# Performance work log

Hardware: AMD Instinct MI355X
Metric: run time of the kernel (lower is better)

The kernel has to match this reference:

```python
import jax, jax.numpy as jnp
import numpy as np

NUM_HEADS = 4
LN_EPS = 1e-5
L2_EPS = 1e-12


def setup_inputs() -> dict:
    key = jax.random.key(0)
    ks = jax.random.split(key, 10)
    B, L, D, Hd = 256, 197, 768, 512
    dh = Hd // NUM_HEADS  # 128
    NC = 1000
    sc = lambda k, shape, s: jax.random.normal(k, shape, jnp.float32) * s
    return {
        "cls_token": jax.random.normal(ks[0], (B, D), jnp.float32),
        "x": jax.random.normal(ks[1], (B, L, D), jnp.float32),
        "proj_w": sc(ks[2], (D, Hd), 0.02),
        "proj_b": jnp.zeros((Hd,), jnp.float32),
        "ln_g": jnp.ones((dh,), jnp.float32),
        "ln_b": jnp.zeros((dh,), jnp.float32),
        "conv1_w": sc(ks[3], (3, 3, 3, 3), 0.2),
        "conv2_w": sc(ks[4], (3, 3, 3, 3), 0.2),
        "cls1_w": sc(ks[5], (D, NC), 0.02),
        "cls1_b": jnp.zeros((NC,), jnp.float32),
        "cls2_w": sc(ks[6], (2883, NC), 0.02),
        "cls2_b": jnp.zeros((NC,), jnp.float32),
    }


def reference(cls_token, x, proj_w, proj_b, ln_g, ln_b, conv1_w, conv2_w,
              cls1_w, cls1_b, cls2_w, cls2_b):
    B, L, D = x.shape
    dh = ln_g.shape[0]
    # proj on patch tokens (drop cls at position 0)
    xp = x[:, 1:, :] @ proj_w + proj_b            # (B, 196, 512)
    Lp = xp.shape[1]
    H = xp.shape[2] // dh
    heads = xp.reshape(B, Lp, H, dh).transpose(2, 0, 1, 3)  # (H, B, Lp, dh)
    # LayerNorm over last dim (eps=1e-5, biased var, affine)
    mu = heads.mean(-1, keepdims=True)
    var = heads.var(-1, keepdims=True)
    hn = (heads - mu) * jax.lax.rsqrt(var + LN_EPS) * ln_g + ln_b
    # Covariance._remove_mean: adaptive_avg_pool2d on (B, dh, Lp) -> mean over BOTH dh and Lp per sample
    hn = hn - hn.mean(axis=(2, 3), keepdims=True)
    # 'near' cross-covariances between adjacent heads, all pairs batched
    x1, x2 = hn[:-1], hn[1:]                      # (H-1, B, Lp, dh)
    cov = jnp.einsum('pbnd,pbne->pbde', x1, x2) / Lp  # (H-1, B, dh, dh)
    # L2 normalize over dim=2 (row axis of each dh x dh map), F.normalize eps
    nrm = jnp.sqrt(jnp.sum(cov * cov, axis=2, keepdims=True))
    cov = cov / jnp.maximum(nrm, L2_EPS)
    cov = cov.transpose(1, 0, 2, 3)               # (B, 3, 128, 128)
    conv = lambda z, w: jax.lax.conv_general_dilated(
        z, w, (2, 2), 'VALID', dimension_numbers=('NCHW', 'OIHW', 'NCHW'))
    z = conv(cov, conv1_w)                        # (B, 3, 63, 63)
    z = jax.nn.gelu(z, approximate=False)
    z = conv(z, conv2_w)                          # (B, 3, 31, 31)
    flat = z.reshape(B, -1)                       # (B, 2883)
    out = ((cls_token @ cls1_w + cls1_b) + (flat @ cls2_w + cls2_b)) / 2
    return out
```

## Files before the change

### kernel.cpp

```cpp
#include <hip/hip_runtime.h>
#include <hip/hip_bf16.h>
#include <cstdint>

typedef __bf16 bf16_t;
typedef __bf16 bf16x4 __attribute__((ext_vector_type(4)));
typedef __bf16 bf16x8 __attribute__((ext_vector_type(8)));
typedef float floatx4 __attribute__((ext_vector_type(4)));

#define LNEPS 1e-5f

__device__ inline void async_copy16(const bf16_t* g, bf16_t* l) {
    __builtin_amdgcn_global_load_lds((const __attribute__((address_space(1))) void*)g,
                                     (__attribute__((address_space(3))) void*)l,
                                     16, 0, 0);
}

__global__ __launch_bounds__(256)
void k_transpose_w(const float* __restrict__ w, bf16_t* __restrict__ wt) {
    __shared__ bf16_t tile[32][33];
    const int bx = blockIdx.x;
    const int by = blockIdx.y;
    const int tx = threadIdx.x & 31, ty = threadIdx.x >> 5;
    for (int i = ty; i < 32; i += 8)
        tile[i][tx] = (bf16_t)w[(by*32 + i)*512 + bx*32 + tx];
    __syncthreads();
    for (int i = ty; i < 32; i += 8)
        wt[(bx*32 + i)*768 + by*32 + tx] = tile[tx][i];
}

__global__ __launch_bounds__(256, 3)
void k_proj_ln(const float* __restrict__ x, const bf16_t* __restrict__ wt,
               const float* __restrict__ pb, const float* __restrict__ lng,
               const float* __restrict__ lnb, bf16_t* __restrict__ hn,
               float* __restrict__ csum)
{
    __shared__ bf16_t As[2][128*32];
    __shared__ bf16_t Bs[2][128*32];

    const int t = threadIdx.x;
    const int lane = t & 63;
    const int wv = t >> 6;
    const int q = lane >> 4;
    const int c = lane & 15;
    const int h  = blockIdx.x;
    const int m0 = blockIdx.y * 128;

    const int arow = t >> 1;
    const int acol = (t & 1) * 16;
    const int agm  = m0 + arow;
    const int ab   = agm / 196;
    const int al   = agm - ab * 196;
    const float* ag = x + ((long)(ab * 197 + al + 1) * 768) + acol;

    const int srow  = t >> 2;
    const int skoff = (t & 3) * 8;
    const bf16_t* bg = wt + (h*128 + srow) * 768 + skoff;

    floatx4 acc[2][8];
#pragma unroll
    for (int i = 0; i < 2; i++)
#pragma unroll
        for (int j = 0; j < 8; j++)
#pragma unroll
            for (int r = 0; r < 4; r++) acc[i][j][r] = 0.f;

    floatx4 a0 = *(const floatx4*)(ag);
    floatx4 a1 = *(const floatx4*)(ag + 4);
    floatx4 a2 = *(const floatx4*)(ag + 8);
    floatx4 a3 = *(const floatx4*)(ag + 12);
    async_copy16(bg,          &Bs[0][t*8]);
    async_copy16(bg + 64*768, &Bs[0][2048 + t*8]);
    {
        bf16x8 w0, w1;
#pragma unroll
        for (int e = 0; e < 4; e++) {
            w0[e] = (bf16_t)a0[e]; w0[e+4] = (bf16_t)a1[e];
            w1[e] = (bf16_t)a2[e]; w1[e+4] = (bf16_t)a3[e];
        }
        *(bf16x8*)&As[0][arow*32 + acol]     = w0;
        *(bf16x8*)&As[0][arow*32 + acol + 8] = w1;
    }
    __syncthreads();

    int buf = 0;
    for (int ks = 0; ks < 24; ks++) {
        const int nbuf = buf ^ 1;
        if (ks < 23) {
            const int kn = (ks + 1) * 32;
            a0 = *(const floatx4*)(ag + kn);
            a1 = *(const floatx4*)(ag + kn + 4);
            a2 = *(const floatx4*)(ag + kn + 8);
            a3 = *(const floatx4*)(ag + kn + 12);
            async_copy16(bg + kn,          &Bs[nbuf][t*8]);
            async_copy16(bg + 64*768 + kn, &Bs[nbuf][2048 + t*8]);
        }
        bf16x8 af[2], bfr[8];
#pragma unroll
        for (int i = 0; i < 2; i++)
            af[i] = *(const bf16x8*)&As[buf][(wv*32 + i*16 + c)*32 + q*8];
#pragma unroll
        for (int j = 0; j < 8; j++)
            bfr[j] = *(const bf16x8*)&Bs[buf][(j*16 + c)*32 + q*8];
#pragma unroll
        for (int i = 0; i < 2; i++)
#pragma unroll
            for (int j = 0; j < 8; j++)
                acc[i][j] = __builtin_amdgcn_mfma_f32_16x16x32_bf16(af[i], bfr[j], acc[i][j], 0, 0, 0);
        if (ks < 23) {
            bf16x8 w0, w1;
#pragma unroll
            for (int e = 0; e < 4; e++) {
                w0[e] = (bf16_t)a0[e]; w0[e+4] = (bf16_t)a1[e];
                w1[e] = (bf16_t)a2[e]; w1[e+4] = (bf16_t)a3[e];
            }
            *(bf16x8*)&As[nbuf][arow*32 + acol]     = w0;
            *(bf16x8*)&As[nbuf][arow*32 + acol + 8] = w1;
        }
        __syncthreads();
        buf = nbuf;
    }

    float bias[8], gg[8], bb[8];
#pragma unroll
    for (int j = 0; j < 8; j++) {
        const int d = j*16 + c;
        bias[j] = pb[h*128 + d];
        gg[j]   = lng[d];
        bb[j]   = lnb[d];
    }
    float cs0[8], cs1[8];
#pragma unroll
    for (int j = 0; j < 8; j++) { cs0[j] = 0.f; cs1[j] = 0.f; }
    const int b0 = m0 / 196;
    const int bL = (m0 + 127) / 196;
#pragma unroll
    for (int i = 0; i < 2; i++) {
#pragma unroll
        for (int r = 0; r < 4; r++) {
            float s = 0.f, s2 = 0.f;
#pragma unroll
            for (int j = 0; j < 8; j++) {
                const float v = acc[i][j][r] + bias[j];
                acc[i][j][r] = v;
                s += v; s2 += v*v;
            }
#pragma unroll
            for (int o = 1; o < 16; o <<= 1) { s += __shfl_xor(s, o); s2 += __shfl_xor(s2, o); }
            const float mu = s * (1.f/128.f);
            const float ms = s2 * (1.f/128.f);
            const float rstd = rsqrtf(ms - mu*mu + LNEPS);
            const int gm = m0 + wv*32 + i*16 + q*4 + r;
            const int bI = gm / 196, l = gm - bI*196;
            bf16_t* dst = hn + (((h*256 + bI)*196 + l) << 7);
            const bool first = (bI == b0);
#pragma unroll
            for (int j = 0; j < 8; j++) {
                const float v = (acc[i][j][r] - mu)*rstd*gg[j] + bb[j];
                dst[j*16 + c] = (bf16_t)v;
                cs0[j] += first ? v : 0.f;
                cs1[j] += first ? 0.f : v;
            }
        }
    }
    float* scr = (float*)As;
#pragma unroll
    for (int j = 0; j < 8; j++) {
        float s0 = cs0[j], s1 = cs1[j];
        s0 += __shfl_xor(s0, 16); s0 += __shfl_xor(s0, 32);
        s1 += __shfl_xor(s1, 16); s1 += __shfl_xor(s1, 32);
        if (q == 0) {
            scr[(wv*2 + 0)*128 + j*16 + c] = s0;
            scr[(wv*2 + 1)*128 + j*16 + c] = s1;
        }
    }
    __syncthreads();
    {
        const int bucket = t >> 7, d = t & 127;
        if (bucket == 0 || bL > b0) {
            const float s = scr[(0*2 + bucket)*128 + d] + scr[(1*2 + bucket)*128 + d]
                          + scr[(2*2 + bucket)*128 + d] + scr[(3*2 + bucket)*128 + d];
            atomicAdd(&csum[((h*256 + b0 + bucket) << 7) + d], s);
        }
    }
}

__global__ __launch_bounds__(256, 2)
void k_cov(const bf16_t* __restrict__ hn, const float* __restrict__ colsum,
           float* __restrict__ cov)
{
    __shared__ bf16_t x1s[128*40];
    __shared__ bf16_t x2s[128*40];
    __shared__ float rs1[128], rs2[128];
    __shared__ float colsq[2][128];
    __shared__ float nrm_inv[128];
    __shared__ float mu_s[2];

    const int t = threadIdx.x;
    const int lane = t & 63;
    const int wv = t >> 6;
    const int wr = wv >> 1, wc = wv & 1;
    const int q = lane >> 4;
    const int c = lane & 15;
    const int b = blockIdx.x;
    const int p = blockIdx.y;

    const bf16_t* X1 = hn + (((p*256 + b)*196) << 7);
    const bf16_t* X2 = hn + ((((p+1)*256 + b)*196) << 7);

    if (t < 128) rs1[t] = colsum[((p*256 + b) << 7) + t];
    else         rs2[t & 127] = colsum[(((p+1)*256 + b) << 7) + (t & 127)];
    __syncthreads();
    if (wv == 0) {
        float s = rs1[lane] + rs1[lane + 64];
#pragma unroll
        for (int o = 1; o < 64; o <<= 1) s += __shfl_xor(s, o);
        if (lane == 0) mu_s[0] = s * (1.f/(196.f*128.f));
    } else if (wv == 1) {
        float s = rs2[lane] + rs2[lane + 64];
#pragma unroll
        for (int o = 1; o < 64; o <<= 1) s += __shfl_xor(s, o);
        if (lane == 0) mu_s[1] = s * (1.f/(196.f*128.f));
    }

    floatx4 acc[4][4];
#pragma unroll
    for (int i = 0; i < 4; i++)
#pragma unroll
        for (int j = 0; j < 4; j++)
#pragma unroll
            for (int r = 0; r < 4; r++) acc[i][j][r] = 0.f;

    const int nl = t >> 3;
    const int d0 = (t & 7) * 16;

    for (int n0 = 0; n0 < 224; n0 += 32) {
        __syncthreads();
        const int n = n0 + nl;
        bf16x8 va, vb, wa, wb;
        if (n < 196) {
            const bf16_t* s1 = X1 + (n << 7) + d0;
            const bf16_t* s2 = X2 + (n << 7) + d0;
            va = *(const bf16x8*)s1;
            vb = *(const bf16x8*)(s1 + 8);
            wa = *(const bf16x8*)s2;
            wb = *(const bf16x8*)(s2 + 8);
        } else {
#pragma unroll
            for (int e = 0; e < 8; e++) {
                va[e] = (bf16_t)0.f; vb[e] = (bf16_t)0.f;
                wa[e] = (bf16_t)0.f; wb[e] = (bf16_t)0.f;
            }
        }
#pragma unroll
        for (int e = 0; e < 8; e++) {
            x1s[(d0 + e)*40 + nl]     = va[e];
            x1s[(d0 + 8 + e)*40 + nl] = vb[e];
            x2s[(d0 + e)*40 + nl]     = wa[e];
            x2s[(d0 + 8 + e)*40 + nl] = wb[e];
        }
        __syncthreads();
        bf16x8 af[4], bfr[4];
#pragma unroll
        for (int i = 0; i < 4; i++)
            af[i] = *(const bf16x8*)&x1s[(wr*64 + i*16 + c)*40 + q*8];
#pragma unroll
        for (int j = 0; j < 4; j++)
            bfr[j] = *(const bf16x8*)&x2s[(wc*64 + j*16 + c)*40 + q*8];
#pragma unroll
        for (int i = 0; i < 4; i++)
#pragma unroll
            for (int j = 0; j < 4; j++)
                acc[i][j] = __builtin_amdgcn_mfma_f32_16x16x32_bf16(af[i], bfr[j], acc[i][j], 0, 0, 0);
    }

    const float mu1 = mu_s[0], mu2 = mu_s[1];
    const float invL = 1.f/196.f;
    float csq[4] = {0.f, 0.f, 0.f, 0.f};
#pragma unroll
    for (int i = 0; i < 4; i++)
#pragma unroll
        for (int j = 0; j < 4; j++)
#pragma unroll
            for (int r = 0; r < 4; r++) {
                const int d = wr*64 + i*16 + q*4 + r;
                const int e = wc*64 + j*16 + c;
                const float v = acc[i][j][r]*invL - mu2*rs1[d]*invL - mu1*rs2[e]*invL + mu1*mu2;
                acc[i][j][r] = v;
                csq[j] += v*v;
            }
#pragma unroll
    for (int j = 0; j < 4; j++) {
        float s = csq[j];
        s += __shfl_xor(s, 16);
        s += __shfl_xor(s, 32);
        csq[j] = s;
    }
    if (q == 0) {
#pragma unroll
        for (int j = 0; j < 4; j++) colsq[wr][wc*64 + j*16 + c] = csq[j];
    }
    __syncthreads();
    if (t < 128) {
        const float nr = sqrtf(colsq[0][t] + colsq[1][t]);
        nrm_inv[t] = 1.f / fmaxf(nr, 1e-12f);
    }
    __syncthreads();
    float* dst = cov + ((long)b*3 + p)*16384;
#pragma unroll
    for (int i = 0; i < 4; i++)
#pragma unroll
        for (int j = 0; j < 4; j++) {
            const int e = wc*64 + j*16 + c;
            const float ni = nrm_inv[e];
#pragma unroll
            for (int r = 0; r < 4; r++) {
                const int d = wr*64 + i*16 + q*4 + r;
                dst[(d << 7) + e] = acc[i][j][r] * ni;
            }
        }
}

__global__ __launch_bounds__(256)
void k_convs(const float* __restrict__ cov, const float* __restrict__ w1,
             const float* __restrict__ w2, bf16_t* __restrict__ Xb)
{
    __shared__ float Z[3*33*63];
    __shared__ float W1s[81];
    __shared__ float W2s[81];
    const int t = threadIdx.x;
    const int b = blockIdx.x >> 1, half = blockIdx.x & 1;
    const int zy0 = half ? 32 : 0;
    const int nzy = half ? 31 : 33;
    const int y20 = half ? 16 : 0;
    const int ny2 = half ? 15 : 16;
    if (t < 81) { W1s[t] = w1[t]; W2s[t] = w2[t]; }
    __syncthreads();
    const float* C = cov + (long)b*3*16384;
    const int ztot = 3*nzy*63;
    for (int idx = t; idx < ztot; idx += 256) {
        const int o = idx / (nzy*63), rem = idx - o*(nzy*63);
        const int yl = rem / 63, xx = rem - yl*63;
        const int y = zy0 + yl;
        float a = 0.f;
#pragma unroll
        for (int i = 0; i < 3; i++) {
            const float* Ci = C + i*16384 + (2*y)*128 + 2*xx;
            const float* Wi = &W1s[o*27 + i*9];
            a += Ci[0]*Wi[0]   + Ci[1]*Wi[1]   + Ci[2]*Wi[2]
               + Ci[128]*Wi[3] + Ci[129]*Wi[4] + Ci[130]*Wi[5]
               + Ci[256]*Wi[6] + Ci[257]*Wi[7] + Ci[258]*Wi[8];
        }
        Z[o*2079 + yl*63 + xx] = 0.5f*a*(1.0f + erff(a*0.70710678118654752f));
    }
    __syncthreads();
    const int c2tot = 3*ny2*31;
    for (int idx = t; idx < c2tot; idx += 256) {
        const int o = idx / (ny2*31), rem = idx - o*(ny2*31);
        const int y2l = rem / 31, x2 = rem - y2l*31;
        float a = 0.f;
#pragma unroll
        for (int i = 0; i < 3; i++) {
            const float* Zi = Z + i*2079 + (2*y2l)*63 + 2*x2;
            const float* Wi = &W2s[(o*3+i)*9];
            a += Zi[0]*Wi[0]   + Zi[1]*Wi[1]   + Zi[2]*Wi[2]
               + Zi[63]*Wi[3]  + Zi[64]*Wi[4]  + Zi[65]*Wi[5]
               + Zi[126]*Wi[6] + Zi[127]*Wi[7] + Zi[128]*Wi[8];
        }
        const int oy2 = y20 + y2l;
        Xb[(long)b*3712 + 768 + o*961 + oy2*31 + x2] = (bf16_t)a;
    }
}

__global__ __launch_bounds__(256)
void k_cvt_cls(const float* __restrict__ cls, bf16_t* __restrict__ Xb,
               float* __restrict__ csum)
{
    const int t = threadIdx.x, b = blockIdx.x;
    for (int k = t; k < 768; k += 256)
        Xb[b*3712 + k] = (bf16_t)cls[b*768 + k];
    if (t < 61) Xb[b*3712 + 3651 + t] = (bf16_t)0.f;
    float* cz = csum + b*512;
    cz[t] = 0.f; cz[t + 256] = 0.f;
}

__global__ __launch_bounds__(256)
void k_cvt_w(const float* __restrict__ W1, const float* __restrict__ W2,
             bf16_t* __restrict__ Wb)
{
    __shared__ bf16_t tile[32][33];
    const int k0 = blockIdx.x * 32;
    const int n0 = blockIdx.y * 32;
    const int tx = threadIdx.x & 31, ty = threadIdx.x >> 5;
    for (int i = ty; i < 32; i += 8) {
        const int k = k0 + i, n = n0 + tx;
        float v = 0.f;
        if (n < 1000 && k < 3651)
            v = (k < 768) ? W1[k*1000 + n] : W2[(k-768)*1000 + n];
        tile[i][tx] = (bf16_t)v;
    }
    __syncthreads();
    for (int i = ty; i < 32; i += 8)
        Wb[(n0 + i)*3712 + k0 + tx] = tile[tx][i];
}

__global__ __launch_bounds__(256, 2)
void k_gemm_cls(const bf16_t* __restrict__ Xb, const bf16_t* __restrict__ Wb,
                float* __restrict__ partial)
{
    __shared__ bf16_t As[128*32];
    __shared__ bf16_t Bs[128*32];

    const int t = threadIdx.x;
    const int lane = t & 63;
    const int wv = t >> 6;
    const int wr = wv >> 1, wc = wv & 1;
    const int q = lane >> 4;
    const int c = lane & 15;
    const int nt = blockIdx.x;
    const int mt = blockIdx.y;
    const int sp = blockIdx.z;

    const int srow  = t >> 2;
    const int skoff = (t & 3) * 8;
    const int m0 = mt * 128, n0 = nt * 128;
    const int kbase = sp * 928;
    const bf16_t* ag0 = Xb + (m0 + srow) * 3712 + kbase + skoff;
    const bf16_t* ag1 = Xb + (m0 + srow + 64) * 3712 + kbase + skoff;
    const bf16_t* bg0 = Wb + (n0 + srow) * 3712 + kbase + skoff;
    const bf16_t* bg1 = Wb + (n0 + srow + 64) * 3712 + kbase + skoff;

    floatx4 acc[4][4];
#pragma unroll
    for (int i = 0; i < 4; i++)
#pragma unroll
        for (int j = 0; j < 4; j++)
#pragma unroll
            for (int r = 0; r < 4; r++) acc[i][j][r] = 0.f;

    for (int k0 = 0; k0 < 928; k0 += 32) {
        __syncthreads();
        async_copy16(ag0 + k0, &As[t*8]);
        async_copy16(ag1 + k0, &As[2048 + t*8]);
        async_copy16(bg0 + k0, &Bs[t*8]);
        async_copy16(bg1 + k0, &Bs[2048 + t*8]);
        __syncthreads();
        bf16x8 af[4], bfr[4];
#pragma unroll
        for (int i = 0; i < 4; i++)
            af[i] = *(const bf16x8*)&As[(wr*64 + i*16 + c)*32 + q*8];
#pragma unroll
        for (int j = 0; j < 4; j++)
            bfr[j] = *(const bf16x8*)&Bs[(wc*64 + j*16 + c)*32 + q*8];
#pragma unroll
        for (int i = 0; i < 4; i++)
#pragma unroll
            for (int j = 0; j < 4; j++)
                acc[i][j] = __builtin_amdgcn_mfma_f32_16x16x32_bf16(af[i], bfr[j], acc[i][j], 0, 0, 0);
    }

    float* base = partial + ((long)sp*256 + m0)*1024 + n0;
#pragma unroll
    for (int i = 0; i < 4; i++)
#pragma unroll
        for (int r = 0; r < 4; r++) {
            const int row = wr*64 + i*16 + q*4 + r;
#pragma unroll
            for (int j = 0; j < 4; j++)
                base[row*1024 + wc*64 + j*16 + c] = acc[i][j][r];
        }
}

__global__ __launch_bounds__(256)
void k_cls_fin(const float* __restrict__ partial, const float* __restrict__ b1,
               const float* __restrict__ b2, float* __restrict__ out)
{
    const int idx = blockIdx.x * 256 + threadIdx.x;
    const int m = idx / 1000, n = idx - m*1000;
    float s = partial[(m)*1024 + n] + partial[(256 + m)*1024 + n]
            + partial[(512 + m)*1024 + n] + partial[(768 + m)*1024 + n];
    out[idx] = 0.5f*(s + b1[n] + b2[n]);
}

extern "C" void kernel_launch(void* const* d_in, const int* in_sizes, int n_in,
                              void* d_out, int out_size, void* d_ws, size_t ws_size,
                              hipStream_t stream) {
    const float* cls = (const float*)d_in[0];
    const float* x   = (const float*)d_in[1];
    const float* pw  = (const float*)d_in[2];
    const float* pb  = (const float*)d_in[3];
    const float* lng = (const float*)d_in[4];
    const float* lnb = (const float*)d_in[5];
    const float* c1w = (const float*)d_in[6];
    const float* c2w = (const float*)d_in[7];
    const float* w1  = (const float*)d_in[8];
    const float* b1  = (const float*)d_in[9];
    const float* w2  = (const float*)d_in[10];
    const float* b2  = (const float*)d_in[11];

    char* ws = (char*)d_ws;
    bf16_t* hn    = (bf16_t*)(ws);
    float*  covb  = (float*) (ws + 51380224ull);
    bf16_t* wt    = (bf16_t*)(ws + 128450560ull);
    float*  csum  = (float*) (ws + 129236992ull);
    bf16_t* Xb    = (bf16_t*)(ws + 129761280ull);
    bf16_t* Wb    = (bf16_t*)(ws + 131661824ull);
    float*  part  = (float*) (ws + 139264000ull);
    float*  out   = (float*)d_out;

    k_transpose_w<<<dim3(16, 24), 256, 0, stream>>>(pw, wt);
    k_cvt_cls<<<256, 256, 0, stream>>>(cls, Xb, csum);
    k_cvt_w<<<dim3(116, 32), 256, 0, stream>>>(w1, w2, Wb);
    k_proj_ln<<<dim3(4, 392), 256, 0, stream>>>(x, wt, pb, lng, lnb, hn, csum);
    k_cov<<<dim3(256, 3), 256, 0, stream>>>(hn, csum, covb);
    k_convs<<<512, 256, 0, stream>>>(covb, c1w, c2w, Xb);
    k_gemm_cls<<<dim3(8, 2, 4), 256, 0, stream>>>(Xb, Wb, part);
    k_cls_fin<<<1000, 256, 0, stream>>>(part, b1, b2, out);
}
```

Measured before the change: 455.7 us.

## Compute all four heads per block in proj+LN so each x row is read once

Each k_proj_ln block now covers 64 token rows and all 512 projection outputs (every head), using 512 threads laid out as an 8-wave 2x4 grid. Previously each x row was fetched from global memory by four separate head blocks. The main loop also changes to a two-stage prefetch with explicit vmcnt/lgkmcnt waits and raw barriers instead of __syncthreads. In exchange, each block streams the whole weight matrix from L2 and uses more LDS, which lowers occupancy, and the column-sum reduction now combines across heads per block.

Result: no change. 447.2 us (-1.9%).

```diff
diff --git a/kernel.cpp b/kernel.cpp
--- a/kernel.cpp
+++ b/kernel.cpp
@@ -28,33 +28,38 @@
         wt[(bx*32 + i)*768 + by*32 + tx] = tile[tx][i];
 }
 
-__global__ __launch_bounds__(256, 3)
+__global__ __launch_bounds__(512, 4)
 void k_proj_ln(const float* __restrict__ x, const bf16_t* __restrict__ wt,
                const float* __restrict__ pb, const float* __restrict__ lng,
                const float* __restrict__ lnb, bf16_t* __restrict__ hn,
                float* __restrict__ csum)
 {
-    __shared__ bf16_t As[2][128*32];
-    __shared__ bf16_t Bs[2][128*32];
+    __shared__ bf16_t As[2][64*32];
+    __shared__ bf16_t Bs[2][512*32];
 
     const int t = threadIdx.x;
     const int lane = t & 63;
     const int wv = t >> 6;
+    const int wr = wv >> 2;
+    const int wc = wv & 3;
     const int q = lane >> 4;
     const int c = lane & 15;
-    const int h  = blockIdx.x;
-    const int m0 = blockIdx.y * 128;
-
-    const int arow = t >> 1;
-    const int acol = (t & 1) * 16;
+    const int m0 = blockIdx.x * 64;
+
+    const int arow = t >> 3;
+    const int acb  = (t & 7) * 4;
     const int agm  = m0 + arow;
     const int ab   = agm / 196;
     const int al   = agm - ab * 196;
-    const float* ag = x + ((long)(ab * 197 + al + 1) * 768) + acol;
-
-    const int srow  = t >> 2;
-    const int skoff = (t & 3) * 8;
-    const bf16_t* bg = wt + (h*128 + srow) * 768 + skoff;
+    const float* ag = x + ((long)(ab * 197 + al + 1) * 768) + acb;
+
+#define BSTAGE(B, kk)                                                          \
+    {                                                                          \
+        _Pragma("unroll")                                                      \
+        for (int m_ = 0; m_ < 4; m_++)                                         \
+            async_copy16(wt + (m_*128 + (t >> 2))*768 + (kk)*32 + (t & 3)*8,   \
+                         &Bs[B][m_*4096 + t*8]);                               \
+    }
 
     floatx4 acc[2][8];
 #pragma unroll
@@ -65,66 +70,71 @@
             for (int r = 0; r < 4; r++) acc[i][j][r] = 0.f;
 
     floatx4 a0 = *(const floatx4*)(ag);
-    floatx4 a1 = *(const floatx4*)(ag + 4);
-    floatx4 a2 = *(const floatx4*)(ag + 8);
-    floatx4 a3 = *(const floatx4*)(ag + 12);
-    async_copy16(bg,          &Bs[0][t*8]);
-    async_copy16(bg + 64*768, &Bs[0][2048 + t*8]);
+    floatx4 a1 = *(const floatx4*)(ag + 32);
+    BSTAGE(0, 0);
+    BSTAGE(1, 1);
     {
-        bf16x8 w0, w1;
-#pragma unroll
-        for (int e = 0; e < 4; e++) {
-            w0[e] = (bf16_t)a0[e]; w0[e+4] = (bf16_t)a1[e];
-            w1[e] = (bf16_t)a2[e]; w1[e+4] = (bf16_t)a3[e];
-        }
-        *(bf16x8*)&As[0][arow*32 + acol]     = w0;
-        *(bf16x8*)&As[0][arow*32 + acol + 8] = w1;
-    }
-    __syncthreads();
-
-    int buf = 0;
-    for (int ks = 0; ks < 24; ks++) {
-        const int nbuf = buf ^ 1;
-        if (ks < 23) {
-            const int kn = (ks + 1) * 32;
-            a0 = *(const floatx4*)(ag + kn);
-            a1 = *(const floatx4*)(ag + kn + 4);
-            a2 = *(const floatx4*)(ag + kn + 8);
-            a3 = *(const floatx4*)(ag + kn + 12);
-            async_copy16(bg + kn,          &Bs[nbuf][t*8]);
-            async_copy16(bg + 64*768 + kn, &Bs[nbuf][2048 + t*8]);
-        }
+        bf16x4 w4;
+#pragma unroll
+        for (int e = 0; e < 4; e++) w4[e] = (bf16_t)a0[e];
+        *(bf16x4*)&As[0][arow*32 + acb] = w4;
+#pragma unroll
+        for (int e = 0; e < 4; e++) w4[e] = (bf16_t)a1[e];
+        *(bf16x4*)&As[1][arow*32 + acb] = w4;
+    }
+
+    floatx4 a_next;
+    for (int ks = 0; ks < 23; ks++) {
+        const int buf = ks & 1;
+        asm volatile("s_waitcnt vmcnt(4)" ::: "memory");
+        asm volatile("s_waitcnt lgkmcnt(0)" ::: "memory");
+        __builtin_amdgcn_s_barrier();
+        if (ks < 22) a_next = *(const floatx4*)(ag + (ks + 2) * 32);
         bf16x8 af[2], bfr[8];
 #pragma unroll
         for (int i = 0; i < 2; i++)
-            af[i] = *(const bf16x8*)&As[buf][(wv*32 + i*16 + c)*32 + q*8];
+            af[i] = *(const bf16x8*)&As[buf][(wr*32 + i*16 + c)*32 + q*8];
 #pragma unroll
         for (int j = 0; j < 8; j++)
-            bfr[j] = *(const bf16x8*)&Bs[buf][(j*16 + c)*32 + q*8];
+            bfr[j] = *(const bf16x8*)&Bs[buf][(wc*128 + j*16 + c)*32 + q*8];
 #pragma unroll
         for (int i = 0; i < 2; i++)
 #pragma unroll
             for (int j = 0; j < 8; j++)
                 acc[i][j] = __builtin_amdgcn_mfma_f32_16x16x32_bf16(af[i], bfr[j], acc[i][j], 0, 0, 0);
-        if (ks < 23) {
-            bf16x8 w0, w1;
-#pragma unroll
-            for (int e = 0; e < 4; e++) {
-                w0[e] = (bf16_t)a0[e]; w0[e+4] = (bf16_t)a1[e];
-                w1[e] = (bf16_t)a2[e]; w1[e+4] = (bf16_t)a3[e];
-            }
-            *(bf16x8*)&As[nbuf][arow*32 + acol]     = w0;
-            *(bf16x8*)&As[nbuf][arow*32 + acol + 8] = w1;
-        }
-        __syncthreads();
-        buf = nbuf;
+        asm volatile("s_waitcnt lgkmcnt(0)" ::: "memory");
+        __builtin_amdgcn_s_barrier();
+        if (ks < 22) {
+            bf16x4 w4;
+#pragma unroll
+            for (int e = 0; e < 4; e++) w4[e] = (bf16_t)a_next[e];
+            *(bf16x4*)&As[buf][arow*32 + acb] = w4;
+            BSTAGE(buf, ks + 2);
+        }
+    }
+    asm volatile("s_waitcnt vmcnt(0)" ::: "memory");
+    asm volatile("s_waitcnt lgkmcnt(0)" ::: "memory");
+    __builtin_amdgcn_s_barrier();
+    {
+        bf16x8 af[2], bfr[8];
+#pragma unroll
+        for (int i = 0; i < 2; i++)
+            af[i] = *(const bf16x8*)&As[1][(wr*32 + i*16 + c)*32 + q*8];
+#pragma unroll
+        for (int j = 0; j < 8; j++)
+            bfr[j] = *(const bf16x8*)&Bs[1][(wc*128 + j*16 + c)*32 + q*8];
+#pragma unroll
+        for (int i = 0; i < 2; i++)
+#pragma unroll
+            for (int j = 0; j < 8; j++)
+                acc[i][j] = __builtin_amdgcn_mfma_f32_16x16x32_bf16(af[i], bfr[j], acc[i][j], 0, 0, 0);
     }
 
     float bias[8], gg[8], bb[8];
 #pragma unroll
     for (int j = 0; j < 8; j++) {
         const int d = j*16 + c;
-        bias[j] = pb[h*128 + d];
+        bias[j] = pb[wc*128 + d];
         gg[j]   = lng[d];
         bb[j]   = lnb[d];
     }
@@ -132,7 +142,7 @@
 #pragma unroll
     for (int j = 0; j < 8; j++) { cs0[j] = 0.f; cs1[j] = 0.f; }
     const int b0 = m0 / 196;
-    const int bL = (m0 + 127) / 196;
+    const int bL = (m0 + 63) / 196;
 #pragma unroll
     for (int i = 0; i < 2; i++) {
 #pragma unroll
@@ -149,9 +159,9 @@
             const float mu = s * (1.f/128.f);
             const float ms = s2 * (1.f/128.f);
             const float rstd = rsqrtf(ms - mu*mu + LNEPS);
-            const int gm = m0 + wv*32 + i*16 + q*4 + r;
+            const int gm = m0 + wr*32 + i*16 + q*4 + r;
             const int bI = gm / 196, l = gm - bI*196;
-            bf16_t* dst = hn + (((h*256 + bI)*196 + l) << 7);
+            bf16_t* dst = hn + (((wc*256 + bI)*196 + l) << 7);
             const bool first = (bI == b0);
 #pragma unroll
             for (int j = 0; j < 8; j++) {
@@ -162,6 +172,7 @@
             }
         }
     }
+    __syncthreads();
     float* scr = (float*)As;
 #pragma unroll
     for (int j = 0; j < 8; j++) {
@@ -175,13 +186,17 @@
     }
     __syncthreads();
     {
-        const int bucket = t >> 7, d = t & 127;
-        if (bucket == 0 || bL > b0) {
-            const float s = scr[(0*2 + bucket)*128 + d] + scr[(1*2 + bucket)*128 + d]
-                          + scr[(2*2 + bucket)*128 + d] + scr[(3*2 + bucket)*128 + d];
-            atomicAdd(&csum[((h*256 + b0 + bucket) << 7) + d], s);
-        }
-    }
+        const int hh = (t >> 7) & 3, d = t & 127;
+#pragma unroll
+        for (int bucket = 0; bucket < 2; bucket++) {
+            if (bucket == 0 || bL > b0) {
+                const float s = scr[(hh*2 + bucket)*128 + d]
+                              + scr[((hh + 4)*2 + bucket)*128 + d];
+                atomicAdd(&csum[((hh*256 + b0 + bucket) << 7) + d], s);
+            }
+        }
+    }
+#undef BSTAGE
 }
 
 __global__ __launch_bounds__(256, 2)
@@ -510,7 +525,7 @@
     k_transpose_w<<<dim3(16, 24), 256, 0, stream>>>(pw, wt);
     k_cvt_cls<<<256, 256, 0, stream>>>(cls, Xb, csum);
     k_cvt_w<<<dim3(116, 32), 256, 0, stream>>>(w1, w2, Wb);
-    k_proj_ln<<<dim3(4, 392), 256, 0, stream>>>(x, wt, pb, lng, lnb, hn, csum);
+    k_proj_ln<<<784, 512, 0, stream>>>(x, wt, pb, lng, lnb, hn, csum);
     k_cov<<<dim3(256, 3), 256, 0, stream>>>(hn, csum, covb);
     k_convs<<<512, 256, 0, stream>>>(covb, c1w, c2w, Xb);
     k_gemm_cls<<<dim3(8, 2, 4), 256, 0, stream>>>(Xb, Wb, part);
```
